# Kernel tuning notes

Hardware: AMD Instinct MI355X
Metric: run time of the kernel (lower is better)

The kernel has to match this reference:

```python
import jax, jax.numpy as jnp
import numpy as np

B, S = 16, 512
VD, TD, H, NH = 768, 768, 1024, 16
HD = H // NH
MAXREL = 128
THRESH = 2.0 / 3.0


def _bitlinear(x, W, b):
    # BitNet b1.58 eval-mode: ternary-quantize weights, rescale, dense matmul
    s = jnp.clip(jnp.mean(jnp.abs(W)), 1e-5, 1000.0)
    wn = jnp.clip(W / s, -10.0, 10.0)
    q = jnp.where(wn > THRESH, 1.0, jnp.where(wn < -THRESH, -1.0, 0.0))
    return x @ (q * s).T + b


def _ln(x, g, b, eps=1e-5):
    m = jnp.mean(x, axis=-1, keepdims=True)
    v = jnp.mean((x - m) ** 2, axis=-1, keepdims=True)
    return (x - m) * jax.lax.rsqrt(v + eps) * g + b


def setup_inputs() -> dict:
    key = jax.random.key(0)
    ks = jax.random.split(key, 10)
    def n(k, shape, std=0.02):
        return jax.random.normal(k, shape, dtype=jnp.float32) * std
    return dict(
        vision_features=jax.random.normal(ks[0], (B, VD), dtype=jnp.float32),
        text_features=jax.random.normal(ks[1], (B, S, TD), dtype=jnp.float32),
        W_vp=n(ks[2], (H, VD)), b_vp=jnp.zeros((H,), jnp.float32),
        W_tp=n(ks[3], (H, TD)), b_tp=jnp.zeros((H,), jnp.float32),
        W_tqkv=n(ks[4], (3 * H, H)), b_tqkv=jnp.zeros((3 * H,), jnp.float32),
        W_vout=n(ks[5], (H, H)), b_vout=jnp.zeros((H,), jnp.float32),
        W_tout=n(ks[6], (H, H)), b_tout=jnp.zeros((H,), jnp.float32),
        g_tn=jnp.ones((H,), jnp.float32), be_tn=jnp.zeros((H,), jnp.float32),
        g_i2t=jnp.ones((H,), jnp.float32), be_i2t=jnp.zeros((H,), jnp.float32),
        g_t2i=jnp.ones((H,), jnp.float32), be_t2i=jnp.zeros((H,), jnp.float32),
        alpha_i2t=jnp.zeros((1,), jnp.float32),
        alpha_t2i=jnp.zeros((1,), jnp.float32),
        rel_embed=n(ks[7], (2 * MAXREL + 1, NH)),
        text_mask=jnp.ones((B, S), dtype=bool),
    )


def reference(vision_features, text_features, W_vp, b_vp, W_tp, b_tp,
              W_tqkv, b_tqkv, W_vout, b_vout, W_tout, b_tout,
              g_tn, be_tn, g_i2t, be_i2t, g_t2i, be_t2i,
              alpha_i2t, alpha_t2i, rel_embed, text_mask):
    scale = HD ** -0.5
    vision_proj = _bitlinear(vision_features, W_vp, b_vp)            # [B,H]
    text_proj = _bitlinear(text_features, W_tp, b_tp)                # [B,S,H]

    # --- text self-attention with relative-position bias ---
    qkv = _bitlinear(_ln(text_proj, g_tn, be_tn), W_tqkv, b_tqkv)    # [B,S,3H]
    qkv = qkv.reshape(B, S, 3, NH, HD).transpose(2, 0, 3, 1, 4)      # [3,B,nh,S,hd]
    q, k, v = qkv[0], qkv[1], qkv[2]
    attn = jnp.einsum('bhqd,bhkd->bhqk', q, k) * scale
    coords = jnp.arange(S)
    rel = jnp.clip(coords[:, None] - coords[None, :], -MAXREL, MAXREL) + MAXREL
    attn = attn + rel_embed[rel].transpose(2, 0, 1)[None]            # +[1,nh,S,S]
    attn = jnp.where(text_mask[:, None, None, :], attn, -1e9)
    attn = jax.nn.softmax(attn, axis=-1)
    text_self = jnp.einsum('bhqk,bhkd->bhqd', attn, v)
    text_self = text_self.transpose(0, 2, 1, 3).reshape(B, S, H)
    text_self = text_proj + text_self                                # residual

    # --- image -> text cross-attention (vision token queries text) ---
    vq = jnp.broadcast_to(vision_proj[:, None], (B, S, H))
    vq = vq.reshape(B, S, NH, HD).transpose(0, 2, 1, 3)              # [B,nh,S,hd]
    tkv = text_self.reshape(B, S, NH, HD).transpose(0, 2, 1, 3)      # [B,nh,S,hd]
    i2t = jnp.einsum('bhqd,bhkd->bhqk', vq, tkv) * scale
    i2t = jnp.where(text_mask[:, None, None, :], i2t, -1e9)
    i2t = jax.nn.softmax(i2t, axis=-1)
    i2t_out = jnp.einsum('bhqk,bhkd->bhqd', i2t, tkv)
    i2t_out = i2t_out.transpose(0, 2, 1, 3).reshape(B, S, H).mean(axis=1)
    i2t_out = _ln(i2t_out, g_i2t, be_i2t)                            # [B,H]
    fused_vision = vision_proj + alpha_i2t * _bitlinear(i2t_out, W_vout, b_vout)

    # --- text -> image cross-attention (text queries single vision token) ---
    tq = text_self.reshape(B, S, NH, HD).transpose(0, 2, 1, 3)       # [B,nh,S,hd]
    vkv = vision_proj.reshape(B, 1, NH, HD).transpose(0, 2, 1, 3)    # [B,nh,1,hd]
    t2i = jnp.einsum('bhqd,bhkd->bhqk', tq, vkv) * scale             # [B,nh,S,1]
    t2i = jax.nn.softmax(t2i, axis=-1)
    t2i_out = jnp.einsum('bhqk,bhkd->bhqd', t2i, vkv)
    t2i_out = t2i_out.transpose(0, 2, 1, 3).reshape(B, S, H)
    t2i_out = _ln(t2i_out, g_t2i, be_t2i)
    fused_text = text_self + alpha_t2i * _bitlinear(t2i_out, W_tout, b_tout)

    return fused_vision, fused_text
```

## Files before the change

### kernel.cpp

```cpp
#include <hip/hip_runtime.h>
#include <cstdint>

#define B_   16
#define S_   512
#define VD_  768
#define TD_  768
#define H_   1024
#define NH_  16
#define HD_  64
#define H3_  3072

typedef __attribute__((ext_vector_type(8))) short bf16x8;
typedef __attribute__((ext_vector_type(4))) float f32x4;

__device__ __forceinline__ float b2f(unsigned short h) {
  union { unsigned u; float f; } x; x.u = ((unsigned)h) << 16; return x.f;
}
__device__ __forceinline__ unsigned short f2b(float f) {
  union { float f; unsigned u; } x; x.f = f;
  unsigned r = x.u + 0x7fffu + ((x.u >> 16) & 1u);
  return (unsigned short)(r >> 16);
}
__device__ __forceinline__ unsigned cvt_pk_bf16(float lo, float hi) {
  unsigned r;
  __asm__("v_cvt_pk_bf16_f32 %0, %1, %2" : "=v"(r) : "v"(lo), "v"(hi));
  return r;
}
__device__ __forceinline__ float fexp2(float x) {
#if __has_builtin(__builtin_amdgcn_exp2f)
  return __builtin_amdgcn_exp2f(x);
#else
  return exp2f(x);
#endif
}

__device__ __forceinline__ void gload_lds16(const void* g, void* lds) {
  __builtin_amdgcn_global_load_lds(
      (const __attribute__((address_space(1))) unsigned int*)g,
      (__attribute__((address_space(3))) unsigned int*)lds, 16, 0, 0);
}
__device__ __forceinline__ void lds_wave_fence() {
  __asm__ __volatile__("s_waitcnt lgkmcnt(0)" ::: "memory");
}

__global__ __launch_bounds__(256) void k_abssum_cvt(const float* __restrict__ w0, int n0,
                                                    const float* __restrict__ w1, int n1,
                                                    const float* __restrict__ w2, int n2,
                                                    const float* __restrict__ w3, int n3,
                                                    const float* __restrict__ w4, int n4,
                                                    double* __restrict__ partials,
                                                    const float* __restrict__ cvt_in,
                                                    unsigned short* __restrict__ cvt_out,
                                                    int cvt_n4) {
  int y = blockIdx.y;
  if (y == 5) {
    for (int i = blockIdx.x * 256 + threadIdx.x; i < cvt_n4; i += 128 * 256) {
      float4 v = ((const float4*)cvt_in)[i];
      ushort4 o; o.x = f2b(v.x); o.y = f2b(v.y); o.z = f2b(v.z); o.w = f2b(v.w);
      ((ushort4*)cvt_out)[i] = o;
    }
    return;
  }
  const float* w = y == 0 ? w0 : y == 1 ? w1 : y == 2 ? w2 : y == 3 ? w3 : w4;
  int n4q = (y == 0 ? n0 : y == 1 ? n1 : y == 2 ? n2 : y == 3 ? n3 : n4) >> 2;
  double s = 0.0;
  for (int i = blockIdx.x * 256 + threadIdx.x; i < n4q; i += 128 * 256) {
    float4 v = ((const float4*)w)[i];
    s += (double)fabsf(v.x) + (double)fabsf(v.y) + (double)fabsf(v.z) + (double)fabsf(v.w);
  }
#pragma unroll
  for (int off = 32; off > 0; off >>= 1) s += __shfl_down(s, off, 64);
  __shared__ double red[4];
  if ((threadIdx.x & 63) == 0) red[threadIdx.x >> 6] = s;
  __syncthreads();
  if (threadIdx.x == 0)
    partials[y * 128 + blockIdx.x] = red[0] + red[1] + red[2] + red[3];
}

__global__ __launch_bounds__(512) void k_sumfin(const double* __restrict__ partials,
                                                double* __restrict__ sums) {
  int wave = threadIdx.x >> 6, lane = threadIdx.x & 63;
  if (wave >= 5) return;
  double s = partials[wave * 128 + lane] + partials[wave * 128 + 64 + lane];
#pragma unroll
  for (int off = 32; off > 0; off >>= 1) s += __shfl_down(s, off, 64);
  if (lane == 0) sums[wave] = s;
}

__global__ __launch_bounds__(256) void k_quant5(const float* __restrict__ w0, int n0,
                                                const float* __restrict__ w1, int n1,
                                                const float* __restrict__ w2, int n2,
                                                const float* __restrict__ w3, int n3,
                                                const float* __restrict__ w4, int n4,
                                                unsigned short* __restrict__ q0,
                                                unsigned short* __restrict__ q1,
                                                unsigned short* __restrict__ q2,
                                                unsigned short* __restrict__ q3,
                                                unsigned short* __restrict__ q4,
                                                const double* __restrict__ sum,
                                                float* __restrict__ s_out) {
  int y = blockIdx.y;
  const float* w = y == 0 ? w0 : y == 1 ? w1 : y == 2 ? w2 : y == 3 ? w3 : w4;
  unsigned short* q = y == 0 ? q0 : y == 1 ? q1 : y == 2 ? q2 : y == 3 ? q3 : q4;
  int n = y == 0 ? n0 : y == 1 ? n1 : y == 2 ? n2 : y == 3 ? n3 : n4;
  double s = fmin(fmax(sum[y] / (double)n, 1e-5), 1000.0);
  if (blockIdx.x == 0 && threadIdx.x == 0) s_out[y] = (float)s;
  int i = blockIdx.x * 256 + threadIdx.x;
  if (i < n) {
    double wn = (double)w[i] / s;
    unsigned short o = 0;
    if (wn > (2.0 / 3.0)) o = 0x3F80u;
    else if (wn < -(2.0 / 3.0)) o = 0xBF80u;
    q[i] = o;
  }
}

__global__ __launch_bounds__(256) void k_rowmat(const float* __restrict__ A,
                                                const unsigned short* __restrict__ W,
                                                const float* __restrict__ sptr,
                                                const float* __restrict__ bias,
                                                float* __restrict__ Cf,
                                                unsigned short* __restrict__ Cb,
                                                const float* __restrict__ resid,
                                                const float* __restrict__ alpha,
                                                int N, int K) {
  const int t = threadIdx.x, lane = t & 63;
  const int w_idx = blockIdx.x * 4 + (t >> 6);
  const int m = w_idx / N, n = w_idx - m * N;
  const int Kper = K >> 6;
  const float* a = A + (size_t)m * K + lane * Kper;
  const unsigned short* w = W + (size_t)n * K + lane * Kper;
  float acc = 0.f;
  for (int k = 0; k < Kper; k += 4) {
    float4 av = *(const float4*)(a + k);
    ushort4 wv = *(const ushort4*)(w + k);
    acc += av.x * b2f(wv.x) + av.y * b2f(wv.y) + av.z * b2f(wv.z) + av.w * b2f(wv.w);
  }
#pragma unroll
  for (int off = 32; off > 0; off >>= 1) acc += __shfl_down(acc, off, 64);
  if (lane == 0) {
    float v = acc * sptr[0] + bias[n];
    if (resid) v = resid[w_idx] + alpha[0] * v;
    Cf[w_idx] = v;
    if (Cb) Cb[w_idx] = f2b(v);
  }
}

__global__ __launch_bounds__(256) void k_ln(const float* __restrict__ x,
                                            const float* __restrict__ g,
                                            const float* __restrict__ be,
                                            float* __restrict__ of,
                                            unsigned short* __restrict__ ob) {
  int row = blockIdx.x, t = threadIdx.x;
  const float4* xr = (const float4*)(x + (size_t)row * H_);
  float4 v = xr[t];
  float s = v.x + v.y + v.z + v.w;
  float s2 = v.x * v.x + v.y * v.y + v.z * v.z + v.w * v.w;
#pragma unroll
  for (int off = 32; off > 0; off >>= 1) { s += __shfl_down(s, off, 64); s2 += __shfl_down(s2, off, 64); }
  __shared__ float rs[4], rs2[4];
  if ((t & 63) == 0) { rs[t >> 6] = s; rs2[t >> 6] = s2; }
  __syncthreads();
  s = rs[0] + rs[1] + rs[2] + rs[3];
  s2 = rs2[0] + rs2[1] + rs2[2] + rs2[3];
  float mean = s * (1.0f / H_);
  float var = s2 * (1.0f / H_) - mean * mean;
  float rstd = rsqrtf(var + 1e-5f);
  const float4 gv = ((const float4*)g)[t];
  const float4 bv = ((const float4*)be)[t];
  float4 o;
  o.x = (v.x - mean) * rstd * gv.x + bv.x;
  o.y = (v.y - mean) * rstd * gv.y + bv.y;
  o.z = (v.z - mean) * rstd * gv.z + bv.z;
  o.w = (v.w - mean) * rstd * gv.w + bv.w;
  if (of) ((float4*)(of + (size_t)row * H_))[t] = o;
  if (ob) {
    ushort4 ou; ou.x = f2b(o.x); ou.y = f2b(o.y); ou.z = f2b(o.z); ou.w = f2b(o.w);
    ((ushort4*)(ob + (size_t)row * H_))[t] = ou;
  }
}

template <int OUTB, int VT>
__global__ __launch_bounds__(256) void k_gemm(const unsigned short* __restrict__ A,
                                              const unsigned short* __restrict__ W,
                                              const float* __restrict__ sptr,
                                              const float* __restrict__ bias,
                                              float* __restrict__ Cf,
                                              unsigned short* __restrict__ Cb,
                                              unsigned short* __restrict__ vt,
                                              int M, int N, int K) {
  __shared__ __align__(16) unsigned short As[2][128 * 64];
  __shared__ __align__(16) unsigned short Bs[2][128 * 64];
  const int t = threadIdx.x, wave = t >> 6, lane = t & 63, quad = lane >> 4, l16 = lane & 15;
  const int bm = blockIdx.y * 128, bn = blockIdx.x * 128;
  const int wm = (wave >> 1) * 64, wn = (wave & 1) * 64;
  const int srow = lane >> 3, kc = (lane & 7) ^ srow;
  f32x4 acc[4][4];
#pragma unroll
  for (int i = 0; i < 4; ++i)
#pragma unroll
    for (int j = 0; j < 4; ++j) acc[i][j] = f32x4{0.f, 0.f, 0.f, 0.f};

  auto stage = [&](int kt, int buf) {
    const int k0 = kt * 64;
#pragma unroll
    for (int c = 0; c < 4; ++c) {
      int row = wave * 32 + c * 8 + srow;
      gload_lds16(A + (size_t)(bm + row) * K + k0 + kc * 8,
                  &As[buf][(wave * 32 + c * 8) * 64]);
      gload_lds16(W + (size_t)(bn + row) * K + k0 + kc * 8,
                  &Bs[buf][(wave * 32 + c * 8) * 64]);
    }
  };

  const int NT = K >> 6;
  stage(0, 0);
  for (int kt = 0; kt < NT; ++kt) {
    const int cur = kt & 1;
    if (kt + 1 < NT) {
      stage(kt + 1, cur ^ 1);
      __asm__ __volatile__("s_waitcnt vmcnt(8)" ::: "memory");
    } else {
      __asm__ __volatile__("s_waitcnt vmcnt(0)" ::: "memory");
    }
    __asm__ __volatile__("s_barrier" ::: "memory");
#pragma unroll
    for (int ks = 0; ks < 2; ++ks) {
      bf16x8 af[4], bfrg[4];
#pragma unroll
      for (int i = 0; i < 4; ++i) {
        int R = wm + i * 16 + l16;
        af[i] = *(const bf16x8*)&As[cur][R * 64 + (((ks * 4 + quad) ^ (R & 7)) * 8)];
      }
#pragma unroll
      for (int j = 0; j < 4; ++j) {
        int R = wn + j * 16 + l16;
        bfrg[j] = *(const bf16x8*)&Bs[cur][R * 64 + (((ks * 4 + quad) ^ (R & 7)) * 8)];
      }
      __builtin_amdgcn_s_setprio(1);
#pragma unroll
      for (int i = 0; i < 4; ++i)
#pragma unroll
        for (int j = 0; j < 4; ++j)
          acc[i][j] = __builtin_amdgcn_mfma_f32_16x16x32_bf16(af[i], bfrg[j], acc[i][j], 0, 0, 0);
      __builtin_amdgcn_s_setprio(0);
    }
    __asm__ __volatile__("s_barrier" ::: "memory");
  }
  float s = sptr[0];

  if (VT && bn >= 2 * H_) {
    unsigned short* T = (wave < 2) ? &As[0][wave * 1152] : &Bs[0][(wave - 2) * 1152];
    const int h = (bn + wn - 2 * H_) >> 6;
    const int b = (bm + wm) >> 9, s0 = (bm + wm) & (S_ - 1);
    const int chunk0 = lane * 2;
#pragma unroll
    for (int j = 0; j < 4; ++j) {
      int n = bn + wn + j * 16 + l16;
      float bv = bias[n];
#pragma unroll
      for (int i = 0; i < 4; ++i)
#pragma unroll
        for (int r = 0; r < 4; ++r)
          T[l16 * 72 + i * 16 + quad * 4 + r] = f2b(acc[i][j][r] * s + bv);
      lds_wave_fence();
#pragma unroll
      for (int cc = 0; cc < 2; ++cc) {
        int ch = chunk0 + cc, dr = ch >> 3, k8 = ch & 7;
        uint4 val = *(const uint4*)&T[dr * 72 + k8 * 8];
        *(uint4*)(vt + ((size_t)(b * NH_ + h) * HD_ + j * 16 + dr) * S_ + s0 + k8 * 8) = val;
      }
      lds_wave_fence();
    }
    return;
  }

#pragma unroll
  for (int j = 0; j < 4; ++j) {
    int n = bn + wn + j * 16 + l16;
    float bv = bias[n];
#pragma unroll
    for (int i = 0; i < 4; ++i) {
#pragma unroll
      for (int r = 0; r < 4; ++r) {
        int m = bm + wm + i * 16 + quad * 4 + r;
        float v = acc[i][j][r] * s + bv;
        if (OUTB) Cb[(size_t)m * N + n] = f2b(v);
        else      Cf[(size_t)m * N + n] = v;
      }
    }
  }
}

__global__ __launch_bounds__(512, 2) void k_flash(const unsigned short* __restrict__ qkv,
                                                  const unsigned short* __restrict__ vt,
                                                  const float* __restrict__ tp,
                                                  const float* __restrict__ rel,
                                                  const float* __restrict__ trow,
                                                  const float* __restrict__ a_t2i,
                                                  float* __restrict__ out_text,
                                                  unsigned short* __restrict__ ts_b) {
  const int h = blockIdx.x, b = blockIdx.y;
  __shared__ __align__(16) unsigned short Ks[2][64 * 64];
  __shared__ __align__(16) unsigned short Vs[2][64 * 64];
  __shared__ __align__(16) unsigned short Ps[8][16 * 72];
  __shared__ float rels[257];
  const int t = threadIdx.x, wave = t >> 6, lane = t & 63, quad = lane >> 4, l16 = lane & 15;
  const int srow = lane >> 3;
  const int kcg = (lane & 7) ^ srow;
  const float LOG2E = 1.4426950408889634f;
  const float SC = 0.125f * LOG2E;

  for (int i = t; i < 257; i += 512) rels[i] = rel[i * NH_ + h] * LOG2E;

  auto stage_kv = [&](int kt, int buf) {
    int row = wave * 8 + srow;
    gload_lds16(qkv + (size_t)(b * S_ + kt * 64 + row) * H3_ + H_ + h * HD_ + kcg * 8,
                &Ks[buf][(wave * 8) * 64]);
    gload_lds16(vt + ((size_t)(b * NH_ + h) * HD_ + row) * S_ + kt * 64 + kcg * 8,
                &Vs[buf][(wave * 8) * 64]);
  };
  auto stageQ = [&](int chunk, unsigned short* buf) {
    int row = chunk * 64 + wave * 8 + srow;
    gload_lds16(qkv + (size_t)(b * S_ + row) * H3_ + h * HD_ + kcg * 8,
                buf + (wave * 8) * 64);
  };

  bf16x8 aq0[4], aq1[4];
  unsigned short* qb0 = &Ks[0][0];
  unsigned short* qb1 = &Vs[0][0];
  unsigned short* qb2 = &Ks[1][0];
  unsigned short* qb3 = &Vs[1][0];
  stageQ(0, qb0); stageQ(1, qb1); stageQ(2, qb2); stageQ(3, qb3);
  __syncthreads();
  if (wave < 4) {
    const unsigned short* qb = wave == 0 ? qb0 : wave == 1 ? qb1 : wave == 2 ? qb2 : qb3;
#pragma unroll
    for (int rg = 0; rg < 4; ++rg) {
      int R = rg * 16 + l16;
      aq0[rg] = *(const bf16x8*)&qb[R * 64 + ((quad ^ (R & 7)) * 8)];
      aq1[rg] = *(const bf16x8*)&qb[R * 64 + (((4 + quad) ^ (R & 7)) * 8)];
    }
  }
  __syncthreads();
  stageQ(4, qb0); stageQ(5, qb1); stageQ(6, qb2); stageQ(7, qb3);
  __syncthreads();
  if (wave >= 4) {
    const int c = wave - 4;
    const unsigned short* qb = c == 0 ? qb0 : c == 1 ? qb1 : c == 2 ? qb2 : qb3;
#pragma unroll
    for (int rg = 0; rg < 4; ++rg) {
      int R = rg * 16 + l16;
      aq0[rg] = *(const bf16x8*)&qb[R * 64 + ((quad ^ (R & 7)) * 8)];
      aq1[rg] = *(const bf16x8*)&qb[R * 64 + (((4 + quad) ^ (R & 7)) * 8)];
    }
  }
  __syncthreads();
  stage_kv(0, 0);

  float mrun[4], lrun[4];
  f32x4 o[4][4];
#pragma unroll
  for (int rg = 0; rg < 4; ++rg) {
    mrun[rg] = -1e30f; lrun[rg] = 0.f;
#pragma unroll
    for (int j = 0; j < 4; ++j) o[rg][j] = f32x4{0.f, 0.f, 0.f, 0.f};
  }

  for (int kt = 0; kt < 8; ++kt) {
    const int cur = kt & 1;
    __syncthreads();
    if (kt < 7) stage_kv(kt + 1, cur ^ 1);

#pragma unroll
    for (int rg = 0; rg < 4; ++rg) {
      const int qb_row = wave * 64 + rg * 16;
      const int dqb = qb_row - kt * 64;
      const bool uni = (dqb >= 192) || (dqb <= -144);
      const float bu = uni ? rels[dqb >= 192 ? 256 : 0] : 0.f;
      const int qg = qb_row + l16;

      float pv[4][4];
#pragma unroll
      for (int j = 0; j < 4; ++j) {
        int R = j * 16 + l16;
        bf16x8 kb0 = *(const bf16x8*)&Ks[cur][R * 64 + ((quad ^ (R & 7)) * 8)];
        bf16x8 kb1 = *(const bf16x8*)&Ks[cur][R * 64 + (((4 + quad) ^ (R & 7)) * 8)];
        f32x4 z = f32x4{0.f, 0.f, 0.f, 0.f};
        z = __builtin_amdgcn_mfma_f32_16x16x32_bf16(kb0, aq0[rg], z, 0, 0, 0);
        z = __builtin_amdgcn_mfma_f32_16x16x32_bf16(kb1, aq1[rg], z, 0, 0, 0);
        if (uni) {
#pragma unroll
          for (int r = 0; r < 4; ++r) pv[j][r] = z[r] * SC + bu;
        } else {
          const int kg0 = kt * 64 + j * 16 + quad * 4;
#pragma unroll
          for (int r = 0; r < 4; ++r) {
            int rix = min(max(qg - kg0 - r, -128), 128) + 128;
            pv[j][r] = z[r] * SC + rels[rix];
          }
        }
      }
      float x = pv[0][0];
#pragma unroll
      for (int j = 0; j < 4; ++j)
#pragma unroll
        for (int r = 0; r < 4; ++r) x = fmaxf(x, pv[j][r]);
      x = fmaxf(x, __shfl_xor(x, 16, 64));
      x = fmaxf(x, __shfl_xor(x, 32, 64));
      if (!__all(x <= mrun[rg])) {
        float mn = fmaxf(mrun[rg], x);
        float al = fexp2(mrun[rg] - mn);
        mrun[rg] = mn;
        lrun[rg] *= al;
        float al0 = __shfl(al, quad * 4 + 0, 64);
        float al1 = __shfl(al, quad * 4 + 1, 64);
        float al2 = __shfl(al, quad * 4 + 2, 64);
        float al3 = __shfl(al, quad * 4 + 3, 64);
#pragma unroll
        for (int jd = 0; jd < 4; ++jd) {
          o[rg][jd][0] *= al0; o[rg][jd][1] *= al1;
          o[rg][jd][2] *= al2; o[rg][jd][3] *= al3;
        }
      }
      float rsum = 0.f;
#pragma unroll
      for (int j = 0; j < 4; ++j)
#pragma unroll
        for (int r = 0; r < 4; ++r) {
          float p = fexp2(pv[j][r] - mrun[rg]);
          pv[j][r] = p;
          rsum += p;
        }
      rsum += __shfl_xor(rsum, 16, 64);
      rsum += __shfl_xor(rsum, 32, 64);
      lrun[rg] += rsum;
      unsigned char* psb = (unsigned char*)&Ps[wave][0] + l16 * 144 + quad * 8;
#pragma unroll
      for (int j = 0; j < 4; ++j) {
        uint2 pk;
        pk.x = cvt_pk_bf16(pv[j][0], pv[j][1]);
        pk.y = cvt_pk_bf16(pv[j][2], pv[j][3]);
        *(uint2*)(psb + j * 32) = pk;
      }
      lds_wave_fence();
#pragma unroll
      for (int ks = 0; ks < 2; ++ks) {
        bf16x8 ap = *(const bf16x8*)&Ps[wave][l16 * 72 + ks * 32 + quad * 8];
#pragma unroll
        for (int jd = 0; jd < 4; ++jd) {
          int R = jd * 16 + l16;
          int C = ks * 4 + quad;
          bf16x8 vb = *(const bf16x8*)&Vs[cur][R * 64 + ((C ^ (R & 7)) * 8)];
          o[rg][jd] = __builtin_amdgcn_mfma_f32_16x16x32_bf16(ap, vb, o[rg][jd], 0, 0, 0);
        }
      }
      lds_wave_fence();
    }
  }
  float a2 = a_t2i[0];
#pragma unroll
  for (int rg = 0; rg < 4; ++rg) {
    float il[4];
#pragma unroll
    for (int r = 0; r < 4; ++r) {
      float lr = __shfl(lrun[rg], quad * 4 + r, 64);
      il[r] = 1.0f / lr;
    }
#pragma unroll
    for (int jd = 0; jd < 4; ++jd) {
#pragma unroll
      for (int r = 0; r < 4; ++r) {
        int g = b * S_ + wave * 64 + rg * 16 + quad * 4 + r;
        int col = h * HD_ + jd * 16 + l16;
        float ov = o[rg][jd][r] * il[r];
        float ts = tp[(size_t)g * H_ + col] + ov;
        ts_b[(size_t)g * H_ + col] = f2b(ts);
        out_text[(size_t)g * H_ + col] = ts + a2 * trow[b * H_ + col];
      }
    }
  }
}

__global__ __launch_bounds__(256) void k_i2t(const unsigned short* __restrict__ vp_b,
                                             const unsigned short* __restrict__ ts_b,
                                             float* __restrict__ i2t_out) {
  const int h = blockIdx.x & 15, b = blockIdx.x >> 4;
  __shared__ float sc[512];
  __shared__ float red[4];
  __shared__ float qv[64];
  __shared__ float ored[4][64];
  const int t = threadIdx.x;
  if (t < 64) qv[t] = b2f(vp_b[b * H_ + h * HD_ + t]);
  __syncthreads();
  for (int k = t; k < 512; k += 256) {
    const unsigned short* kr = ts_b + (size_t)(b * S_ + k) * H_ + h * HD_;
    float acc = 0.f;
#pragma unroll
    for (int dc = 0; dc < 8; ++dc) {
      uint4 u = *(const uint4*)(kr + dc * 8);
      const unsigned short* p = (const unsigned short*)&u;
#pragma unroll
      for (int i = 0; i < 8; ++i) acc += qv[dc * 8 + i] * b2f(p[i]);
    }
    sc[k] = acc * 0.125f;
  }
  __syncthreads();
  float m = -1e30f;
  for (int k = t; k < 512; k += 256) m = fmaxf(m, sc[k]);
#pragma unroll
  for (int off = 1; off < 64; off <<= 1) m = fmaxf(m, __shfl_xor(m, off, 64));
  if ((t & 63) == 0) red[t >> 6] = m;
  __syncthreads();
  m = fmaxf(fmaxf(red[0], red[1]), fmaxf(red[2], red[3]));
  __syncthreads();
  float ls = 0.f;
  for (int k = t; k < 512; k += 256) { float p = __expf(sc[k] - m); sc[k] = p; ls += p; }
#pragma unroll
  for (int off = 1; off < 64; off <<= 1) ls += __shfl_xor(ls, off, 64);
  if ((t & 63) == 0) red[t >> 6] = ls;
  __syncthreads();
  float tot = red[0] + red[1] + red[2] + red[3];
  const int d = t & 63, grp = t >> 6;
  float acc = 0.f;
  for (int k = grp; k < 512; k += 4)
    acc += sc[k] * b2f(ts_b[(size_t)(b * S_ + k) * H_ + h * HD_ + d]);
  ored[grp][d] = acc;
  __syncthreads();
  if (t < 64)
    i2t_out[b * H_ + h * HD_ + t] = (ored[0][t] + ored[1][t] + ored[2][t] + ored[3][t]) / tot;
}

extern "C" void kernel_launch(void* const* d_in, const int* in_sizes, int n_in,
                              void* d_out, int out_size, void* d_ws, size_t ws_size,
                              hipStream_t stream) {
  const float* vf     = (const float*)d_in[0];
  const float* tf     = (const float*)d_in[1];
  const float* W_vp   = (const float*)d_in[2];
  const float* b_vp   = (const float*)d_in[3];
  const float* W_tp   = (const float*)d_in[4];
  const float* b_tp   = (const float*)d_in[5];
  const float* W_tqkv = (const float*)d_in[6];
  const float* b_tqkv = (const float*)d_in[7];
  const float* W_vout = (const float*)d_in[8];
  const float* b_vout = (const float*)d_in[9];
  const float* W_tout = (const float*)d_in[10];
  const float* b_tout = (const float*)d_in[11];
  const float* g_tn   = (const float*)d_in[12];
  const float* be_tn  = (const float*)d_in[13];
  const float* g_i2t  = (const float*)d_in[14];
  const float* be_i2t = (const float*)d_in[15];
  const float* g_t2i  = (const float*)d_in[16];
  const float* be_t2i = (const float*)d_in[17];
  const float* a_i2t  = (const float*)d_in[18];
  const float* a_t2i  = (const float*)d_in[19];
  const float* rel    = (const float*)d_in[20];

  size_t off = 0;
  auto alloc = [&](size_t bytes) -> void* {
    void* p = (char*)d_ws + off;
    off += (bytes + 255) & ~(size_t)255;
    return p;
  };
  double* sums     = (double*)alloc(64);
  double* partials = (double*)alloc(5 * 128 * 8);
  float* scales    = (float*)alloc(64);
  unsigned short* q_vp   = (unsigned short*)alloc((size_t)H_ * VD_ * 2);
  unsigned short* q_tp   = (unsigned short*)alloc((size_t)H_ * TD_ * 2);
  unsigned short* q_tqkv = (unsigned short*)alloc((size_t)H3_ * H_ * 2);
  unsigned short* q_vout = (unsigned short*)alloc((size_t)H_ * H_ * 2);
  unsigned short* q_tout = (unsigned short*)alloc((size_t)H_ * H_ * 2);
  unsigned short* tf_b   = (unsigned short*)alloc((size_t)B_ * S_ * TD_ * 2);
  float* text_proj       = (float*)alloc((size_t)B_ * S_ * H_ * 4);
  unsigned short* ln_tp  = (unsigned short*)alloc((size_t)B_ * S_ * H_ * 2);
  unsigned short* qkv    = (unsigned short*)alloc((size_t)B_ * S_ * H3_ * 2);
  unsigned short* vt     = (unsigned short*)alloc((size_t)B_ * NH_ * HD_ * S_ * 2);
  unsigned short* ts_b   = (unsigned short*)alloc((size_t)B_ * S_ * H_ * 2);
  float* vision_proj     = (float*)alloc((size_t)B_ * H_ * 4);
  unsigned short* vp_b   = (unsigned short*)alloc((size_t)B_ * H_ * 2);
  float* ln_t2i_f        = (float*)alloc((size_t)B_ * H_ * 4);
  float* trow            = (float*)alloc((size_t)B_ * H_ * 4);
  float* i2t_out         = (float*)alloc((size_t)B_ * H_ * 4);
  float* ln_i2t_f        = (float*)alloc((size_t)B_ * H_ * 4);

  float* out_vision = (float*)d_out;
  float* out_text   = (float*)d_out + B_ * H_;

  k_abssum_cvt<<<dim3(128, 6), 256, 0, stream>>>(W_vp, H_ * VD_, W_tp, H_ * TD_,
                                                 W_tqkv, H3_ * H_, W_vout, H_ * H_,
                                                 W_tout, H_ * H_, partials,
                                                 tf, tf_b, B_ * S_ * TD_ / 4);
  k_sumfin<<<1, 512, 0, stream>>>(partials, sums);
  k_quant5<<<dim3((H3_ * H_ + 255) / 256, 5), 256, 0, stream>>>(
      W_vp, H_ * VD_, W_tp, H_ * TD_, W_tqkv, H3_ * H_, W_vout, H_ * H_, W_tout, H_ * H_,
      q_vp, q_tp, q_tqkv, q_vout, q_tout, sums, scales);

  k_rowmat<<<(B_ * H_) / 4, 256, 0, stream>>>(vf, q_vp, scales + 0, b_vp,
                                              vision_proj, vp_b, nullptr, nullptr, H_, VD_);
  k_ln<<<B_, 256, 0, stream>>>(vision_proj, g_t2i, be_t2i, ln_t2i_f, nullptr);
  k_rowmat<<<(B_ * H_) / 4, 256, 0, stream>>>(ln_t2i_f, q_tout, scales + 4, b_tout,
                                              trow, nullptr, nullptr, nullptr, H_, H_);

  k_gemm<0, 0><<<dim3(H_ / 128, (B_ * S_) / 128), 256, 0, stream>>>(
      tf_b, q_tp, scales + 1, b_tp, text_proj, nullptr, nullptr, B_ * S_, H_, TD_);
  k_ln<<<B_ * S_, 256, 0, stream>>>(text_proj, g_tn, be_tn, nullptr, ln_tp);
  k_gemm<1, 1><<<dim3(H3_ / 128, (B_ * S_) / 128), 256, 0, stream>>>(
      ln_tp, q_tqkv, scales + 2, b_tqkv, nullptr, qkv, vt, B_ * S_, H3_, H_);
  k_flash<<<dim3(NH_, B_), 512, 0, stream>>>(qkv, vt, text_proj, rel, trow, a_t2i,
                                             out_text, ts_b);
  k_i2t<<<B_ * NH_, 256, 0, stream>>>(vp_b, ts_b, i2t_out);
  k_ln<<<B_, 256, 0, stream>>>(i2t_out, g_i2t, be_i2t, ln_i2t_f, nullptr);
  k_rowmat<<<(B_ * H_) / 4, 256, 0, stream>>>(ln_i2t_f, q_vout, scales + 3, b_vout,
                                              out_vision, nullptr, vision_proj, a_i2t, H_, H_);
}
```

Before: 369.9 us.

## Fuse vision-path matvecs and layernorm, fold i2t attention into flash kernel

The separate sum-finalize kernel is removed: each quantization block now reduces the abs-sum partials itself. The vision projection, its layernorm and the text-out matvec are merged into one 1024-thread kernel per batch row, and the i2t layernorm plus output matvec are merged the same way. The image-to-text attention is moved into the flash kernel's epilogue, which keeps the per-head text-self tile in LDS, so the bf16 text_self buffer is no longer written to and re-read from global memory. The cost is far fewer launches and less global traffic, but the vision matvecs now run on only 16 blocks with per-thread strided weight-row reads. The flash kernel also uses much more LDS.

Result: slower. 501.1 us (+35.5%).

```diff
diff --git a/kernel.cpp b/kernel.cpp
--- a/kernel.cpp
+++ b/kernel.cpp
@@ -77,16 +77,6 @@
     partials[y * 128 + blockIdx.x] = red[0] + red[1] + red[2] + red[3];
 }
 
-__global__ __launch_bounds__(512) void k_sumfin(const double* __restrict__ partials,
-                                                double* __restrict__ sums) {
-  int wave = threadIdx.x >> 6, lane = threadIdx.x & 63;
-  if (wave >= 5) return;
-  double s = partials[wave * 128 + lane] + partials[wave * 128 + 64 + lane];
-#pragma unroll
-  for (int off = 32; off > 0; off >>= 1) s += __shfl_down(s, off, 64);
-  if (lane == 0) sums[wave] = s;
-}
-
 __global__ __launch_bounds__(256) void k_quant5(const float* __restrict__ w0, int n0,
                                                 const float* __restrict__ w1, int n1,
                                                 const float* __restrict__ w2, int n2,
@@ -97,15 +87,24 @@
                                                 unsigned short* __restrict__ q2,
                                                 unsigned short* __restrict__ q3,
                                                 unsigned short* __restrict__ q4,
-                                                const double* __restrict__ sum,
+                                                const double* __restrict__ partials,
                                                 float* __restrict__ s_out) {
   int y = blockIdx.y;
   const float* w = y == 0 ? w0 : y == 1 ? w1 : y == 2 ? w2 : y == 3 ? w3 : w4;
   unsigned short* q = y == 0 ? q0 : y == 1 ? q1 : y == 2 ? q2 : y == 3 ? q3 : q4;
   int n = y == 0 ? n0 : y == 1 ? n1 : y == 2 ? n2 : y == 3 ? n3 : n4;
-  double s = fmin(fmax(sum[y] / (double)n, 1e-5), 1000.0);
-  if (blockIdx.x == 0 && threadIdx.x == 0) s_out[y] = (float)s;
-  int i = blockIdx.x * 256 + threadIdx.x;
+  const int t = threadIdx.x;
+  __shared__ double sbc;
+  if (t < 64) {
+    double sv = partials[y * 128 + t] + partials[y * 128 + 64 + t];
+#pragma unroll
+    for (int off = 32; off > 0; off >>= 1) sv += __shfl_down(sv, off, 64);
+    if (t == 0) sbc = sv;
+  }
+  __syncthreads();
+  double s = fmin(fmax(sbc / (double)n, 1e-5), 1000.0);
+  if (blockIdx.x == 0 && t == 0) s_out[y] = (float)s;
+  int i = blockIdx.x * 256 + t;
   if (i < n) {
     double wn = (double)w[i] / s;
     unsigned short o = 0;
@@ -115,35 +114,91 @@
   }
 }
 
-__global__ __launch_bounds__(256) void k_rowmat(const float* __restrict__ A,
-                                                const unsigned short* __restrict__ W,
-                                                const float* __restrict__ sptr,
-                                                const float* __restrict__ bias,
-                                                float* __restrict__ Cf,
-                                                unsigned short* __restrict__ Cb,
-                                                const float* __restrict__ resid,
-                                                const float* __restrict__ alpha,
-                                                int N, int K) {
-  const int t = threadIdx.x, lane = t & 63;
-  const int w_idx = blockIdx.x * 4 + (t >> 6);
-  const int m = w_idx / N, n = w_idx - m * N;
-  const int Kper = K >> 6;
-  const float* a = A + (size_t)m * K + lane * Kper;
-  const unsigned short* w = W + (size_t)n * K + lane * Kper;
+__global__ __launch_bounds__(1024) void k_vision(const float* __restrict__ vf,
+                                                 const unsigned short* __restrict__ q_vp,
+                                                 const unsigned short* __restrict__ q_tout,
+                                                 const float* __restrict__ scales,
+                                                 const float* __restrict__ b_vp,
+                                                 const float* __restrict__ b_tout,
+                                                 const float* __restrict__ g_t2i,
+                                                 const float* __restrict__ be_t2i,
+                                                 float* __restrict__ vision_proj,
+                                                 unsigned short* __restrict__ vp_b,
+                                                 float* __restrict__ trow) {
+  const int b = blockIdx.x, t = threadIdx.x, wave = t >> 6, lane = t & 63;
+  __shared__ float xrow[VD_];
+  __shared__ float lnrow[H_];
+  __shared__ float rs[16], rs2[16];
+  if (t < VD_) xrow[t] = vf[b * VD_ + t];
+  __syncthreads();
   float acc = 0.f;
-  for (int k = 0; k < Kper; k += 4) {
-    float4 av = *(const float4*)(a + k);
+  const unsigned short* w = q_vp + (size_t)t * VD_;
+  for (int k = 0; k < VD_; k += 4) {
+    float4 xv = *(const float4*)&xrow[k];
     ushort4 wv = *(const ushort4*)(w + k);
-    acc += av.x * b2f(wv.x) + av.y * b2f(wv.y) + av.z * b2f(wv.z) + av.w * b2f(wv.w);
-  }
-#pragma unroll
-  for (int off = 32; off > 0; off >>= 1) acc += __shfl_down(acc, off, 64);
-  if (lane == 0) {
-    float v = acc * sptr[0] + bias[n];
-    if (resid) v = resid[w_idx] + alpha[0] * v;
-    Cf[w_idx] = v;
-    if (Cb) Cb[w_idx] = f2b(v);
-  }
+    acc += xv.x * b2f(wv.x) + xv.y * b2f(wv.y) + xv.z * b2f(wv.z) + xv.w * b2f(wv.w);
+  }
+  float vp = acc * scales[0] + b_vp[t];
+  vision_proj[b * H_ + t] = vp;
+  vp_b[b * H_ + t] = f2b(vp);
+  float s = vp, s2 = vp * vp;
+#pragma unroll
+  for (int off = 32; off > 0; off >>= 1) { s += __shfl_down(s, off, 64); s2 += __shfl_down(s2, off, 64); }
+  if (lane == 0) { rs[wave] = s; rs2[wave] = s2; }
+  __syncthreads();
+  float ts_ = 0.f, ts2_ = 0.f;
+#pragma unroll
+  for (int wv = 0; wv < 16; ++wv) { ts_ += rs[wv]; ts2_ += rs2[wv]; }
+  float mean = ts_ * (1.0f / H_);
+  float var = ts2_ * (1.0f / H_) - mean * mean;
+  float rstd = rsqrtf(var + 1e-5f);
+  lnrow[t] = (vp - mean) * rstd * g_t2i[t] + be_t2i[t];
+  __syncthreads();
+  float acc2 = 0.f;
+  const unsigned short* w2 = q_tout + (size_t)t * H_;
+  for (int k = 0; k < H_; k += 4) {
+    float4 xv = *(const float4*)&lnrow[k];
+    ushort4 wv = *(const ushort4*)(w2 + k);
+    acc2 += xv.x * b2f(wv.x) + xv.y * b2f(wv.y) + xv.z * b2f(wv.z) + xv.w * b2f(wv.w);
+  }
+  trow[b * H_ + t] = acc2 * scales[4] + b_tout[t];
+}
+
+__global__ __launch_bounds__(1024) void k_vfinal(const float* __restrict__ i2t_out,
+                                                 const unsigned short* __restrict__ q_vout,
+                                                 const float* __restrict__ scales,
+                                                 const float* __restrict__ b_vout,
+                                                 const float* __restrict__ g_i2t,
+                                                 const float* __restrict__ be_i2t,
+                                                 const float* __restrict__ vision_proj,
+                                                 const float* __restrict__ a_i2t,
+                                                 float* __restrict__ out_vision) {
+  const int b = blockIdx.x, t = threadIdx.x, wave = t >> 6, lane = t & 63;
+  __shared__ float lnrow[H_];
+  __shared__ float rs[16], rs2[16];
+  float x = i2t_out[b * H_ + t];
+  float s = x, s2 = x * x;
+#pragma unroll
+  for (int off = 32; off > 0; off >>= 1) { s += __shfl_down(s, off, 64); s2 += __shfl_down(s2, off, 64); }
+  if (lane == 0) { rs[wave] = s; rs2[wave] = s2; }
+  __syncthreads();
+  float ts_ = 0.f, ts2_ = 0.f;
+#pragma unroll
+  for (int wv = 0; wv < 16; ++wv) { ts_ += rs[wv]; ts2_ += rs2[wv]; }
+  float mean = ts_ * (1.0f / H_);
+  float var = ts2_ * (1.0f / H_) - mean * mean;
+  float rstd = rsqrtf(var + 1e-5f);
+  lnrow[t] = (x - mean) * rstd * g_i2t[t] + be_i2t[t];
+  __syncthreads();
+  float acc = 0.f;
+  const unsigned short* w = q_vout + (size_t)t * H_;
+  for (int k = 0; k < H_; k += 4) {
+    float4 xv = *(const float4*)&lnrow[k];
+    ushort4 wv = *(const ushort4*)(w + k);
+    acc += xv.x * b2f(wv.x) + xv.y * b2f(wv.y) + xv.z * b2f(wv.z) + xv.w * b2f(wv.w);
+  }
+  float v = acc * scales[3] + b_vout[t];
+  out_vision[b * H_ + t] = vision_proj[b * H_ + t] + a_i2t[0] * v;
 }
 
 __global__ __launch_bounds__(256) void k_ln(const float* __restrict__ x,
@@ -298,13 +353,19 @@
                                                   const float* __restrict__ rel,
                                                   const float* __restrict__ trow,
                                                   const float* __restrict__ a_t2i,
+                                                  const unsigned short* __restrict__ vp_b,
                                                   float* __restrict__ out_text,
-                                                  unsigned short* __restrict__ ts_b) {
+                                                  float* __restrict__ i2t_out) {
   const int h = blockIdx.x, b = blockIdx.y;
   __shared__ __align__(16) unsigned short Ks[2][64 * 64];
   __shared__ __align__(16) unsigned short Vs[2][64 * 64];
   __shared__ __align__(16) unsigned short Ps[8][16 * 72];
+  __shared__ __align__(16) unsigned short TS[512][68];
   __shared__ float rels[257];
+  __shared__ float qvs[64];
+  __shared__ float scs[512];
+  __shared__ float redm[8], redl[8];
+  __shared__ float ored[8][64];
   const int t = threadIdx.x, wave = t >> 6, lane = t & 63, quad = lane >> 4, l16 = lane & 15;
   const int srow = lane >> 3;
   const int kcg = (lane & 7) ^ srow;
@@ -312,6 +373,7 @@
   const float SC = 0.125f * LOG2E;
 
   for (int i = t; i < 257; i += 512) rels[i] = rel[i * NH_ + h] * LOG2E;
+  if (t < 64) qvs[t] = b2f(vp_b[b * H_ + h * HD_ + t]);
 
   auto stage_kv = [&](int kt, int buf) {
     int row = wave * 8 + srow;
@@ -471,64 +533,54 @@
     for (int jd = 0; jd < 4; ++jd) {
 #pragma unroll
       for (int r = 0; r < 4; ++r) {
-        int g = b * S_ + wave * 64 + rg * 16 + quad * 4 + r;
+        int sl = wave * 64 + rg * 16 + quad * 4 + r;
+        int g = b * S_ + sl;
         int col = h * HD_ + jd * 16 + l16;
         float ov = o[rg][jd][r] * il[r];
         float ts = tp[(size_t)g * H_ + col] + ov;
-        ts_b[(size_t)g * H_ + col] = f2b(ts);
+        TS[sl][jd * 16 + l16] = f2b(ts);
         out_text[(size_t)g * H_ + col] = ts + a2 * trow[b * H_ + col];
       }
     }
   }
-}
-
-__global__ __launch_bounds__(256) void k_i2t(const unsigned short* __restrict__ vp_b,
-                                             const unsigned short* __restrict__ ts_b,
-                                             float* __restrict__ i2t_out) {
-  const int h = blockIdx.x & 15, b = blockIdx.x >> 4;
-  __shared__ float sc[512];
-  __shared__ float red[4];
-  __shared__ float qv[64];
-  __shared__ float ored[4][64];
-  const int t = threadIdx.x;
-  if (t < 64) qv[t] = b2f(vp_b[b * H_ + h * HD_ + t]);
-  __syncthreads();
-  for (int k = t; k < 512; k += 256) {
-    const unsigned short* kr = ts_b + (size_t)(b * S_ + k) * H_ + h * HD_;
-    float acc = 0.f;
-#pragma unroll
-    for (int dc = 0; dc < 8; ++dc) {
-      uint4 u = *(const uint4*)(kr + dc * 8);
-      const unsigned short* p = (const unsigned short*)&u;
-#pragma unroll
-      for (int i = 0; i < 8; ++i) acc += qv[dc * 8 + i] * b2f(p[i]);
-    }
-    sc[k] = acc * 0.125f;
-  }
-  __syncthreads();
-  float m = -1e30f;
-  for (int k = t; k < 512; k += 256) m = fmaxf(m, sc[k]);
+  __syncthreads();
+
+  const int grp = t >> 6, d = t & 63;
+  float a = 0.f;
+#pragma unroll
+  for (int dc = 0; dc < 16; ++dc) {
+    uint2 u = *(const uint2*)&TS[t][dc * 4];
+    const unsigned short* p = (const unsigned short*)&u;
+    a += qvs[dc * 4 + 0] * b2f(p[0]) + qvs[dc * 4 + 1] * b2f(p[1])
+       + qvs[dc * 4 + 2] * b2f(p[2]) + qvs[dc * 4 + 3] * b2f(p[3]);
+  }
+  float sc0 = a * 0.125f;
+  float m = sc0;
 #pragma unroll
   for (int off = 1; off < 64; off <<= 1) m = fmaxf(m, __shfl_xor(m, off, 64));
-  if ((t & 63) == 0) red[t >> 6] = m;
-  __syncthreads();
-  m = fmaxf(fmaxf(red[0], red[1]), fmaxf(red[2], red[3]));
-  __syncthreads();
-  float ls = 0.f;
-  for (int k = t; k < 512; k += 256) { float p = __expf(sc[k] - m); sc[k] = p; ls += p; }
+  if (lane == 0) redm[wave] = m;
+  __syncthreads();
+  m = redm[0];
+#pragma unroll
+  for (int wv = 1; wv < 8; ++wv) m = fmaxf(m, redm[wv]);
+  float p = __expf(sc0 - m);
+  scs[t] = p;
+  float ls = p;
 #pragma unroll
   for (int off = 1; off < 64; off <<= 1) ls += __shfl_xor(ls, off, 64);
-  if ((t & 63) == 0) red[t >> 6] = ls;
-  __syncthreads();
-  float tot = red[0] + red[1] + red[2] + red[3];
-  const int d = t & 63, grp = t >> 6;
+  if (lane == 0) redl[wave] = ls;
+  __syncthreads();
+  float tot = redl[0] + redl[1] + redl[2] + redl[3] + redl[4] + redl[5] + redl[6] + redl[7];
   float acc = 0.f;
-  for (int k = grp; k < 512; k += 4)
-    acc += sc[k] * b2f(ts_b[(size_t)(b * S_ + k) * H_ + h * HD_ + d]);
+  for (int k = grp; k < 512; k += 8)
+    acc += scs[k] * b2f(TS[k][d]);
   ored[grp][d] = acc;
   __syncthreads();
-  if (t < 64)
-    i2t_out[b * H_ + h * HD_ + t] = (ored[0][t] + ored[1][t] + ored[2][t] + ored[3][t]) / tot;
+  if (t < 64) {
+    float o8 = ored[0][t] + ored[1][t] + ored[2][t] + ored[3][t]
+             + ored[4][t] + ored[5][t] + ored[6][t] + ored[7][t];
+    i2t_out[b * H_ + h * HD_ + t] = o8 / tot;
+  }
 }
 
 extern "C" void kernel_launch(void* const* d_in, const int* in_sizes, int n_in,
@@ -562,7 +614,6 @@
     off += (bytes + 255) & ~(size_t)255;
     return p;
   };
-  double* sums     = (double*)alloc(64);
   double* partials = (double*)alloc(5 * 128 * 8);
   float* scales    = (float*)alloc(64);
   unsigned short* q_vp   = (unsigned short*)alloc((size_t)H_ * VD_ * 2);
@@ -575,13 +626,10 @@
   unsigned short* ln_tp  = (unsigned short*)alloc((size_t)B_ * S_ * H_ * 2);
   unsigned short* qkv    = (unsigned short*)alloc((size_t)B_ * S_ * H3_ * 2);
   unsigned short* vt     = (unsigned short*)alloc((size_t)B_ * NH_ * HD_ * S_ * 2);
-  unsigned short* ts_b   = (unsigned short*)alloc((size_t)B_ * S_ * H_ * 2);
   float* vision_proj     = (float*)alloc((size_t)B_ * H_ * 4);
   unsigned short* vp_b   = (unsigned short*)alloc((size_t)B_ * H_ * 2);
-  float* ln_t2i_f        = (float*)alloc((size_t)B_ * H_ * 4);
   float* trow            = (float*)alloc((size_t)B_ * H_ * 4);
   float* i2t_out         = (float*)alloc((size_t)B_ * H_ * 4);
-  float* ln_i2t_f        = (float*)alloc((size_t)B_ * H_ * 4);
 
   float* out_vision = (float*)d_out;
   float* out_text   = (float*)d_out + B_ * H_;
@@ -590,16 +638,12 @@
                                                  W_tqkv, H3_ * H_, W_vout, H_ * H_,
                                                  W_tout, H_ * H_, partials,
                                                  tf, tf_b, B_ * S_ * TD_ / 4);
-  k_sumfin<<<1, 512, 0, stream>>>(partials, sums);
   k_quant5<<<dim3((H3_ * H_ + 255) / 256, 5), 256, 0, stream>>>(
       W_vp, H_ * VD_, W_tp, H_ * TD_, W_tqkv, H3_ * H_, W_vout, H_ * H_, W_tout, H_ * H_,
-      q_vp, q_tp, q_tqkv, q_vout, q_tout, sums, scales);
-
-  k_rowmat<<<(B_ * H_) / 4, 256, 0, stream>>>(vf, q_vp, scales + 0, b_vp,
-                                              vision_proj, vp_b, nullptr, nullptr, H_, VD_);
-  k_ln<<<B_, 256, 0, stream>>>(vision_proj, g_t2i, be_t2i, ln_t2i_f, nullptr);
-  k_rowmat<<<(B_ * H_) / 4, 256, 0, stream>>>(ln_t2i_f, q_tout, scales + 4, b_tout,
-                                              trow, nullptr, nullptr, nullptr, H_, H_);
+      q_vp, q_tp, q_tqkv, q_vout, q_tout, partials, scales);
+
+  k_vision<<<B_, 1024, 0, stream>>>(vf, q_vp, q_tout, scales, b_vp, b_tout,
+                                    g_t2i, be_t2i, vision_proj, vp_b, trow);
 
   k_gemm<0, 0><<<dim3(H_ / 128, (B_ * S_) / 128), 256, 0, stream>>>(
       tf_b, q_tp, scales + 1, b_tp, text_proj, nullptr, nullptr, B_ * S_, H_, TD_);
@@ -607,9 +651,7 @@
   k_gemm<1, 1><<<dim3(H3_ / 128, (B_ * S_) / 128), 256, 0, stream>>>(
       ln_tp, q_tqkv, scales + 2, b_tqkv, nullptr, qkv, vt, B_ * S_, H3_, H_);
   k_flash<<<dim3(NH_, B_), 512, 0, stream>>>(qkv, vt, text_proj, rel, trow, a_t2i,
-                                             out_text, ts_b);
-  k_i2t<<<B_ * NH_, 256, 0, stream>>>(vp_b, ts_b, i2t_out);
-  k_ln<<<B_, 256, 0, stream>>>(i2t_out, g_i2t, be_i2t, ln_i2t_f, nullptr);
-  k_rowmat<<<(B_ * H_) / 4, 256, 0, stream>>>(ln_i2t_f, q_vout, scales + 3, b_vout,
-                                              out_vision, nullptr, vision_proj, a_i2t, H_, H_);
-}
+                                             vp_b, out_text, i2t_out);
+  k_vfinal<<<B_, 1024, 0, stream>>>(i2t_out, q_vout, scales, b_vout, g_i2t, be_i2t,
+                                    vision_proj, a_i2t, out_vision);
+}
```

## Fuse image-to-text attention into flash epilogue and sum finalize into quant

Applied to the files above, without the earlier changes.

Each flash block now stages its bf16 text_self head slice in a large LDS tile and computes the single-query image-to-text attention in place. This removes the separate k_i2t kernel and the global ts_b round trip. The abs-sum finalization is folded into the quantization kernel, with each block reducing the partials itself, which drops one launch. The extra ~70KB of LDS per flash block may reduce occupancy.

New measurement: 358.5 us. -3.1%, faster.

```diff
diff --git a/kernel.cpp b/kernel.cpp
--- a/kernel.cpp
+++ b/kernel.cpp
@@ -77,16 +77,6 @@
     partials[y * 128 + blockIdx.x] = red[0] + red[1] + red[2] + red[3];
 }
 
-__global__ __launch_bounds__(512) void k_sumfin(const double* __restrict__ partials,
-                                                double* __restrict__ sums) {
-  int wave = threadIdx.x >> 6, lane = threadIdx.x & 63;
-  if (wave >= 5) return;
-  double s = partials[wave * 128 + lane] + partials[wave * 128 + 64 + lane];
-#pragma unroll
-  for (int off = 32; off > 0; off >>= 1) s += __shfl_down(s, off, 64);
-  if (lane == 0) sums[wave] = s;
-}
-
 __global__ __launch_bounds__(256) void k_quant5(const float* __restrict__ w0, int n0,
                                                 const float* __restrict__ w1, int n1,
                                                 const float* __restrict__ w2, int n2,
@@ -97,15 +87,24 @@
                                                 unsigned short* __restrict__ q2,
                                                 unsigned short* __restrict__ q3,
                                                 unsigned short* __restrict__ q4,
-                                                const double* __restrict__ sum,
+                                                const double* __restrict__ partials,
                                                 float* __restrict__ s_out) {
   int y = blockIdx.y;
   const float* w = y == 0 ? w0 : y == 1 ? w1 : y == 2 ? w2 : y == 3 ? w3 : w4;
   unsigned short* q = y == 0 ? q0 : y == 1 ? q1 : y == 2 ? q2 : y == 3 ? q3 : q4;
   int n = y == 0 ? n0 : y == 1 ? n1 : y == 2 ? n2 : y == 3 ? n3 : n4;
-  double s = fmin(fmax(sum[y] / (double)n, 1e-5), 1000.0);
-  if (blockIdx.x == 0 && threadIdx.x == 0) s_out[y] = (float)s;
-  int i = blockIdx.x * 256 + threadIdx.x;
+  const int t = threadIdx.x;
+  __shared__ double sbc;
+  if (t < 64) {
+    double sv = partials[y * 128 + t] + partials[y * 128 + 64 + t];
+#pragma unroll
+    for (int off = 32; off > 0; off >>= 1) sv += __shfl_down(sv, off, 64);
+    if (t == 0) sbc = sv;
+  }
+  __syncthreads();
+  double s = fmin(fmax(sbc / (double)n, 1e-5), 1000.0);
+  if (blockIdx.x == 0 && t == 0) s_out[y] = (float)s;
+  int i = blockIdx.x * 256 + t;
   if (i < n) {
     double wn = (double)w[i] / s;
     unsigned short o = 0;
@@ -298,13 +297,19 @@
                                                   const float* __restrict__ rel,
                                                   const float* __restrict__ trow,
                                                   const float* __restrict__ a_t2i,
+                                                  const unsigned short* __restrict__ vp_b,
                                                   float* __restrict__ out_text,
-                                                  unsigned short* __restrict__ ts_b) {
+                                                  float* __restrict__ i2t_out) {
   const int h = blockIdx.x, b = blockIdx.y;
   __shared__ __align__(16) unsigned short Ks[2][64 * 64];
   __shared__ __align__(16) unsigned short Vs[2][64 * 64];
   __shared__ __align__(16) unsigned short Ps[8][16 * 72];
+  __shared__ __align__(16) unsigned short TS[512][68];
   __shared__ float rels[257];
+  __shared__ float qvs[64];
+  __shared__ float scs[512];
+  __shared__ float redm[8], redl[8];
+  __shared__ float ored[8][64];
   const int t = threadIdx.x, wave = t >> 6, lane = t & 63, quad = lane >> 4, l16 = lane & 15;
   const int srow = lane >> 3;
   const int kcg = (lane & 7) ^ srow;
@@ -312,6 +317,7 @@
   const float SC = 0.125f * LOG2E;
 
   for (int i = t; i < 257; i += 512) rels[i] = rel[i * NH_ + h] * LOG2E;
+  if (t < 64) qvs[t] = b2f(vp_b[b * H_ + h * HD_ + t]);
 
   auto stage_kv = [&](int kt, int buf) {
     int row = wave * 8 + srow;
@@ -471,64 +477,54 @@
     for (int jd = 0; jd < 4; ++jd) {
 #pragma unroll
       for (int r = 0; r < 4; ++r) {
-        int g = b * S_ + wave * 64 + rg * 16 + quad * 4 + r;
+        int sl = wave * 64 + rg * 16 + quad * 4 + r;
+        int g = b * S_ + sl;
         int col = h * HD_ + jd * 16 + l16;
         float ov = o[rg][jd][r] * il[r];
         float ts = tp[(size_t)g * H_ + col] + ov;
-        ts_b[(size_t)g * H_ + col] = f2b(ts);
+        TS[sl][jd * 16 + l16] = f2b(ts);
         out_text[(size_t)g * H_ + col] = ts + a2 * trow[b * H_ + col];
       }
     }
   }
-}
-
-__global__ __launch_bounds__(256) void k_i2t(const unsigned short* __restrict__ vp_b,
-                                             const unsigned short* __restrict__ ts_b,
-                                             float* __restrict__ i2t_out) {
-  const int h = blockIdx.x & 15, b = blockIdx.x >> 4;
-  __shared__ float sc[512];
-  __shared__ float red[4];
-  __shared__ float qv[64];
-  __shared__ float ored[4][64];
-  const int t = threadIdx.x;
-  if (t < 64) qv[t] = b2f(vp_b[b * H_ + h * HD_ + t]);
-  __syncthreads();
-  for (int k = t; k < 512; k += 256) {
-    const unsigned short* kr = ts_b + (size_t)(b * S_ + k) * H_ + h * HD_;
-    float acc = 0.f;
-#pragma unroll
-    for (int dc = 0; dc < 8; ++dc) {
-      uint4 u = *(const uint4*)(kr + dc * 8);
-      const unsigned short* p = (const unsigned short*)&u;
-#pragma unroll
-      for (int i = 0; i < 8; ++i) acc += qv[dc * 8 + i] * b2f(p[i]);
-    }
-    sc[k] = acc * 0.125f;
-  }
-  __syncthreads();
-  float m = -1e30f;
-  for (int k = t; k < 512; k += 256) m = fmaxf(m, sc[k]);
+  __syncthreads();
+
+  const int grp = t >> 6, d = t & 63;
+  float a = 0.f;
+#pragma unroll
+  for (int dc = 0; dc < 16; ++dc) {
+    uint2 u = *(const uint2*)&TS[t][dc * 4];
+    const unsigned short* p = (const unsigned short*)&u;
+    a += qvs[dc * 4 + 0] * b2f(p[0]) + qvs[dc * 4 + 1] * b2f(p[1])
+       + qvs[dc * 4 + 2] * b2f(p[2]) + qvs[dc * 4 + 3] * b2f(p[3]);
+  }
+  float sc0 = a * 0.125f;
+  float m = sc0;
 #pragma unroll
   for (int off = 1; off < 64; off <<= 1) m = fmaxf(m, __shfl_xor(m, off, 64));
-  if ((t & 63) == 0) red[t >> 6] = m;
-  __syncthreads();
-  m = fmaxf(fmaxf(red[0], red[1]), fmaxf(red[2], red[3]));
-  __syncthreads();
-  float ls = 0.f;
-  for (int k = t; k < 512; k += 256) { float p = __expf(sc[k] - m); sc[k] = p; ls += p; }
+  if (lane == 0) redm[wave] = m;
+  __syncthreads();
+  m = redm[0];
+#pragma unroll
+  for (int wv = 1; wv < 8; ++wv) m = fmaxf(m, redm[wv]);
+  float p = __expf(sc0 - m);
+  scs[t] = p;
+  float ls = p;
 #pragma unroll
   for (int off = 1; off < 64; off <<= 1) ls += __shfl_xor(ls, off, 64);
-  if ((t & 63) == 0) red[t >> 6] = ls;
-  __syncthreads();
-  float tot = red[0] + red[1] + red[2] + red[3];
-  const int d = t & 63, grp = t >> 6;
+  if (lane == 0) redl[wave] = ls;
+  __syncthreads();
+  float tot = redl[0] + redl[1] + redl[2] + redl[3] + redl[4] + redl[5] + redl[6] + redl[7];
   float acc = 0.f;
-  for (int k = grp; k < 512; k += 4)
-    acc += sc[k] * b2f(ts_b[(size_t)(b * S_ + k) * H_ + h * HD_ + d]);
+  for (int k = grp; k < 512; k += 8)
+    acc += scs[k] * b2f(TS[k][d]);
   ored[grp][d] = acc;
   __syncthreads();
-  if (t < 64)
-    i2t_out[b * H_ + h * HD_ + t] = (ored[0][t] + ored[1][t] + ored[2][t] + ored[3][t]) / tot;
+  if (t < 64) {
+    float o8 = ored[0][t] + ored[1][t] + ored[2][t] + ored[3][t]
+             + ored[4][t] + ored[5][t] + ored[6][t] + ored[7][t];
+    i2t_out[b * H_ + h * HD_ + t] = o8 / tot;
+  }
 }
 
 extern "C" void kernel_launch(void* const* d_in, const int* in_sizes, int n_in,
@@ -562,7 +558,6 @@
     off += (bytes + 255) & ~(size_t)255;
     return p;
   };
-  double* sums     = (double*)alloc(64);
   double* partials = (double*)alloc(5 * 128 * 8);
   float* scales    = (float*)alloc(64);
   unsigned short* q_vp   = (unsigned short*)alloc((size_t)H_ * VD_ * 2);
@@ -575,7 +570,6 @@
   unsigned short* ln_tp  = (unsigned short*)alloc((size_t)B_ * S_ * H_ * 2);
   unsigned short* qkv    = (unsigned short*)alloc((size_t)B_ * S_ * H3_ * 2);
   unsigned short* vt     = (unsigned short*)alloc((size_t)B_ * NH_ * HD_ * S_ * 2);
-  unsigned short* ts_b   = (unsigned short*)alloc((size_t)B_ * S_ * H_ * 2);
   float* vision_proj     = (float*)alloc((size_t)B_ * H_ * 4);
   unsigned short* vp_b   = (unsigned short*)alloc((size_t)B_ * H_ * 2);
   float* ln_t2i_f        = (float*)alloc((size_t)B_ * H_ * 4);
@@ -590,10 +584,9 @@
                                                  W_tqkv, H3_ * H_, W_vout, H_ * H_,
                                                  W_tout, H_ * H_, partials,
                                                  tf, tf_b, B_ * S_ * TD_ / 4);
-  k_sumfin<<<1, 512, 0, stream>>>(partials, sums);
   k_quant5<<<dim3((H3_ * H_ + 255) / 256, 5), 256, 0, stream>>>(
       W_vp, H_ * VD_, W_tp, H_ * TD_, W_tqkv, H3_ * H_, W_vout, H_ * H_, W_tout, H_ * H_,
-      q_vp, q_tp, q_tqkv, q_vout, q_tout, sums, scales);
+      q_vp, q_tp, q_tqkv, q_vout, q_tout, partials, scales);
 
   k_rowmat<<<(B_ * H_) / 4, 256, 0, stream>>>(vf, q_vp, scales + 0, b_vp,
                                               vision_proj, vp_b, nullptr, nullptr, H_, VD_);
@@ -607,8 +600,7 @@
   k_gemm<1, 1><<<dim3(H3_ / 128, (B_ * S_) / 128), 256, 0, stream>>>(
       ln_tp, q_tqkv, scales + 2, b_tqkv, nullptr, qkv, vt, B_ * S_, H3_, H_);
   k_flash<<<dim3(NH_, B_), 512, 0, stream>>>(qkv, vt, text_proj, rel, trow, a_t2i,
-                                             out_text, ts_b);
-  k_i2t<<<B_ * NH_, 256, 0, stream>>>(vp_b, ts_b, i2t_out);
+                                             vp_b, out_text, i2t_out);
   k_ln<<<B_, 256, 0, stream>>>(i2t_out, g_i2t, be_i2t, ln_i2t_f, nullptr);
   k_rowmat<<<(B_ * H_) / 4, 256, 0, stream>>>(ln_i2t_f, q_vout, scales + 3, b_vout,
                                               out_vision, nullptr, vision_proj, a_i2t, H_, H_);
```
